# Performance work log

Measured on AMD Instinct MI355X. Metric: run time of the kernel, lower is better.

The kernel has to match this reference:

```python
import jax, jax.numpy as jnp
import numpy as np

KS = 3          # kernel size (forced by the view() shape constraint)
STRIDE = 1
PAD = 1
DIL = 1
K = KS * KS     # 9 taps


def _bilinear_sample(x, py, px):
    """x: [B,C,Hin,Win]; py,px: [B,C,K,H,W] float sample coords.
    Zero padding outside bounds (torchvision DeformConv semantics:
    each corner contributes only if it lies inside the image)."""
    B, C, Hin, Win = x.shape
    y0 = jnp.floor(py)
    x0 = jnp.floor(px)
    wy1 = py - y0
    wx1 = px - x0
    wy0 = 1.0 - wy1
    wx0 = 1.0 - wx1
    xf = x.reshape(B, C, Hin * Win)

    def gather(yi, xi):
        valid = (yi >= 0) & (yi <= Hin - 1) & (xi >= 0) & (xi <= Win - 1)
        yc = jnp.clip(yi, 0, Hin - 1).astype(jnp.int32)
        xc = jnp.clip(xi, 0, Win - 1).astype(jnp.int32)
        flat = (yc * Win + xc).reshape(B, C, -1)
        g = jnp.take_along_axis(xf, flat, axis=2).reshape(yi.shape)
        return jnp.where(valid, g, 0.0)

    return (wy0 * wx0 * gather(y0, x0)
            + wy0 * wx1 * gather(y0, x0 + 1)
            + wy1 * wx0 * gather(y0 + 1, x0)
            + wy1 * wx1 * gather(y0 + 1, x0 + 1))


def setup_inputs() -> dict:
    key = jax.random.key(0)
    ks = jax.random.split(key, 5)
    B, C, H, W = 8, 64, 128, 128
    Cout = 64
    return {
        "x": jax.random.normal(ks[0], (B, C, H, W), dtype=jnp.float32),
        # depthwise offset conv: groups=C, out = 18*C -> weight (18C, 1, 3, 3)
        "offset_w": jax.random.normal(ks[1], (2 * K * C, 1, 3, 3), dtype=jnp.float32) * 0.05,
        "offset_b": jax.random.normal(ks[2], (2 * K * C,), dtype=jnp.float32) * 0.05,
        "deform_w": jax.random.normal(ks[3], (Cout, C, KS, KS), dtype=jnp.float32) * 0.05,
        "deform_b": jax.random.normal(ks[4], (Cout,), dtype=jnp.float32) * 0.05,
    }


def reference(x, offset_w, offset_b, deform_w, deform_b):
    B, C, H, W = x.shape
    Cout = deform_w.shape[0]

    # 1) depthwise offset conv (groups = in_channels)
    off = jax.lax.conv_general_dilated(
        x, offset_w, window_strides=(STRIDE, STRIDE),
        padding=((PAD, PAD), (PAD, PAD)), rhs_dilation=(DIL, DIL),
        feature_group_count=C,
        dimension_numbers=("NCHW", "OIHW", "NCHW"))
    off = off + offset_b[None, :, None, None]

    # 2) softmax over the full channel axis (dim=1 in torch)
    off = jax.nn.softmax(off, axis=1)

    # 3) torchvision offset layout: channel 2*(g*K + k) + {0:dy, 1:dx},
    #    deformable_groups = C (per-input-channel offsets)
    off = off.reshape(B, C, K, 2, H, W)
    dy = off[:, :, :, 0]   # [B,C,K,H,W]
    dx = off[:, :, :, 1]

    base_y = (jnp.arange(H, dtype=x.dtype) * STRIDE - PAD)   # [H]
    base_x = (jnp.arange(W, dtype=x.dtype) * STRIDE - PAD)   # [W]
    ky = (jnp.repeat(jnp.arange(KS), KS) * DIL).astype(x.dtype)  # [K]
    kx = (jnp.tile(jnp.arange(KS), KS) * DIL).astype(x.dtype)

    py = base_y[None, None, None, :, None] + ky[None, None, :, None, None] + dy
    px = base_x[None, None, None, None, :] + kx[None, None, :, None, None] + dx

    sampled = _bilinear_sample(x, py, px)                    # [B,C,K,H,W]

    # 4) weighted accumulation over (c_in, kernel tap)
    out = jnp.einsum("bckhw,ock->bohw", sampled, deform_w.reshape(Cout, C, K))
    return out + deform_b[None, :, None, None]
```

## Files before the change

### kernel.cpp

```cpp
#include <hip/hip_runtime.h>

#define B_    8
#define C_    64
#define H_    128
#define W_    128
#define K_    9
#define J_    18
#define COUT_ 64
#define TPX   16
#define CK    576
#define SROW  584
#define NW81  (C_ * 81)
#define L2E   1.4426950408889634f

typedef __attribute__((ext_vector_type(8))) short short8;
typedef __attribute__((ext_vector_type(4))) float float4v;
typedef __attribute__((ext_vector_type(2))) float f32x2;

__device__ __forceinline__ unsigned short f2bf(float f) {
    unsigned int u = __float_as_uint(f);
    u = u + 0x7fffu + ((u >> 16) & 1u);
    return (unsigned short)(u >> 16);
}

constexpr int TMAP[9] = {0, 1, 2, 7, 8, 9, 14, 15, 16};

__global__ __launch_bounds__(256)
void nchw_to_nhwc(const float* __restrict__ x, float* __restrict__ xt) {
    __shared__ float tile[64][65];
    const int bid = blockIdx.x;
    const int wt  = bid & 1;
    const int h   = (bid >> 1) & 127;
    const int b   = bid >> 8;
    const int w0  = wt << 6;
    const int q   = threadIdx.x >> 6;
    const int l   = threadIdx.x & 63;
    #pragma unroll
    for (int r = 0; r < 16; r++) {
        const int c = q * 16 + r;
        tile[c][l] = x[((size_t)(b * C_ + c) * H_ + h) * W_ + w0 + l];
    }
    __syncthreads();
    #pragma unroll
    for (int r = 0; r < 16; r++) {
        const int w = q * 16 + r;
        xt[((size_t)(b * H_ + h) * W_ + w0 + w) * C_ + l] = tile[l][w];
    }
}

__global__ __launch_bounds__(256)
void prep_weights(const float* __restrict__ dw, unsigned short* __restrict__ dwb,
                  const float* __restrict__ ow, unsigned int* __restrict__ owp) {
    const int bid = blockIdx.x;
    const int dwblocks = (CK * COUT_) / 256;
    if (bid < dwblocks) {
        const int i = bid * 256 + threadIdx.x;
        dwb[i] = f2bf(dw[i]);
    } else {
        const int i = (bid - dwblocks) * 256 + threadIdx.x;
        if (i < NW81) {
            const int c = i / 81, r = i - c * 81;
            const int k = r / 9,  t = r - k * 9;
            const float* s = ow + c * 162 + k * 18 + t;
            owp[i] = (unsigned int)f2bf(s[0] * L2E) |
                     ((unsigned int)f2bf(s[9] * L2E) << 16);
        }
    }
}

template<int T>
__device__ __forceinline__ void conv_steps(const unsigned int* __restrict__ owc,
                                           const float (&S)[28], f32x2 (&v2)[4][9]) {
    if constexpr (T < 81) {
        const unsigned int pw = owc[T];
        const f32x2 w2 = {__uint_as_float(pw << 16),
                          __uint_as_float(pw & 0xffff0000u)};
        constexpr int k = T / 9;
        constexpr int p = TMAP[T % 9];
        #pragma unroll
        for (int px = 0; px < 4; px++) {
            const float s = S[p + px];
            v2[px][k] = __builtin_elementwise_fma(w2, (f32x2){s, s}, v2[px][k]);
        }
        conv_steps<T + 1>(owc, S, v2);
    }
}

template<int I>
__device__ __forceinline__ void taps_px(const f32x2 (&w)[9], const float inv,
                                        const float (&S)[28],
                                        unsigned short* __restrict__ sb) {
    #pragma unroll
    for (int k = 0; k < 9; k++) {
        const float dy = w[k].x * inv;
        const float dx = w[k].y * inv;
        const int base = TMAP[k] + I;
        const float a  = S[base],     bb = S[base + 1];
        const float c  = S[base + 7], dd = S[base + 8];
        const float top = fmaf(dx, bb - a, a);
        const float bot = fmaf(dx, dd - c, c);
        sb[k] = f2bf(fmaf(dy, bot - top, top));
    }
}

template<bool NHWC, bool PREB, bool PREP>
__global__ __launch_bounds__(256, 3)
void dcn_fused(const float* __restrict__ xsrc,
               const float* __restrict__ ow,
               const unsigned int* __restrict__ owp,
               const float* __restrict__ ob,
               const float* __restrict__ dw,
               const unsigned short* __restrict__ dwb,
               const float* __restrict__ db,
               float* __restrict__ out) {
    static_assert(TPX * SROW * sizeof(unsigned short) <= NW81 * sizeof(unsigned int), "union");
    __shared__ __align__(16) unsigned int smem[NW81];
    unsigned int* ow_s = smem;
    unsigned short* sbuf = (unsigned short*)smem;

    const int tid  = threadIdx.x;
    const int wave = tid >> 6;
    const int lane = tid & 63;

    const int bid = blockIdx.x;
    const int b   = bid >> 10;
    const int rem = bid & 1023;
    const int h   = rem >> 3;
    const int w0  = (rem & 7) << 4;

    if (PREP) {
        #pragma unroll
        for (int i = 0; i < 21; i++) {
            const int idx = tid + i * 256;
            if (idx < NW81) ow_s[idx] = owp[idx];
        }
    } else {
        for (int i = tid; i < NW81; i += 256) {
            const int c = i / 81, r = i - c * 81;
            const int k = r / 9,  t = r - k * 9;
            const float* s = ow + c * 162 + k * 18 + t;
            ow_s[i] = (unsigned int)f2bf(s[0] * L2E) |
                      ((unsigned int)f2bf(s[9] * L2E) << 16);
        }
    }
    __syncthreads();

    const int wbase = w0 + (wave << 2);
    const unsigned int* owc = ow_s + lane * 81;

    float S[28];
    if (h >= 1 && h <= H_ - 3 && wbase >= 1 && wbase <= W_ - 6) {
        const float* p0 = NHWC
            ? xsrc + ((size_t)(b * H_ + (h - 1)) * W_ + (wbase - 1)) * C_ + lane
            : xsrc + ((size_t)(b * C_ + lane) * H_ + (h - 1)) * W_ + (wbase - 1);
        const int rs = NHWC ? (W_ * C_) : W_;
        const int cs = NHWC ? C_ : 1;
        #pragma unroll
        for (int r = 0; r < 4; r++)
            #pragma unroll
            for (int s = 0; s < 7; s++)
                S[r * 7 + s] = p0[r * rs + s * cs];
    } else {
        #pragma unroll
        for (int r = 0; r < 4; r++) {
            const int y = h - 1 + r;
            const bool yv = (unsigned)y < (unsigned)H_;
            #pragma unroll
            for (int s = 0; s < 7; s++) {
                const int xx = wbase - 1 + s;
                const bool ok = yv && ((unsigned)xx < (unsigned)W_);
                const float* p = NHWC
                    ? xsrc + ((size_t)(b * H_ + (y & 127)) * W_ + (xx & 127)) * C_ + lane
                    : xsrc + ((size_t)(b * C_ + lane) * H_ + (y & 127)) * W_ + (xx & 127);
                S[r * 7 + s] = ok ? *p : 0.0f;
            }
        }
    }

    f32x2 v2[4][9];
    const float2* obp = (const float2*)(ob + lane * J_);
    #pragma unroll
    for (int p = 0; p < 9; p++) {
        const float2 f = obp[p];
        const f32x2 b2 = {f.x * L2E, f.y * L2E};
        v2[0][p] = b2; v2[1][p] = b2; v2[2][p] = b2; v2[3][p] = b2;
    }
    conv_steps<0>(owc, S, v2);

    float psum[4];
    #pragma unroll
    for (int px = 0; px < 4; px++) {
        float s = 0.0f;
        #pragma unroll
        for (int k = 0; k < 9; k++) {
            f32x2 e;
            e.x = __builtin_amdgcn_exp2f(v2[px][k].x);
            e.y = __builtin_amdgcn_exp2f(v2[px][k].y);
            v2[px][k] = e;
            s += e.x + e.y;
        }
        psum[px] = s;
    }

    __syncthreads();

    #pragma unroll
    for (int px = 0; px < 4; px++) psum[px] += __shfl_xor(psum[px], 32, 64);
#define RED_LEVEL(PAT) do { \
        const float r0_ = __uint_as_float((unsigned)__builtin_amdgcn_ds_swizzle((int)__float_as_uint(psum[0]), (PAT))); \
        const float r1_ = __uint_as_float((unsigned)__builtin_amdgcn_ds_swizzle((int)__float_as_uint(psum[1]), (PAT))); \
        const float r2_ = __uint_as_float((unsigned)__builtin_amdgcn_ds_swizzle((int)__float_as_uint(psum[2]), (PAT))); \
        const float r3_ = __uint_as_float((unsigned)__builtin_amdgcn_ds_swizzle((int)__float_as_uint(psum[3]), (PAT))); \
        psum[0] += r0_; psum[1] += r1_; psum[2] += r2_; psum[3] += r3_; \
    } while (0)
    RED_LEVEL(0x401F);
    RED_LEVEL(0x201F);
    RED_LEVEL(0x101F);
    RED_LEVEL(0x081F);
    RED_LEVEL(0x041F);
#undef RED_LEVEL

    const float inv0 = __builtin_amdgcn_rcpf(psum[0]);
    const float inv1 = __builtin_amdgcn_rcpf(psum[1]);
    const float inv2 = __builtin_amdgcn_rcpf(psum[2]);
    const float inv3 = __builtin_amdgcn_rcpf(psum[3]);

    unsigned short* sb = sbuf + (wave << 2) * SROW + lane * K_;
    taps_px<0>(v2[0], inv0, S, sb);
    taps_px<1>(v2[1], inv1, S, sb + SROW);
    taps_px<2>(v2[2], inv2, S, sb + 2 * SROW);
    taps_px<3>(v2[3], inv3, S, sb + 3 * SROW);

    __syncthreads();

    const int quad = lane >> 4;
    const int o    = (wave << 4) + (lane & 15);
    float4v acc = {0.f, 0.f, 0.f, 0.f};
    const unsigned short* arow = sbuf + (lane & 15) * SROW + quad * 8;
    #pragma unroll
    for (int t = 0; t < 18; t++) {
        short8 afrag = *(const short8*)(arow + t * 32);
        short8 bfrag;
        if (PREB) {
            bfrag = *(const short8*)(dwb + (size_t)o * CK + quad * 8 + t * 32);
        } else {
            const float* brow = dw + (size_t)o * CK + quad * 8 + t * 32;
            float4 b0 = *(const float4*)brow;
            float4 b1 = *(const float4*)(brow + 4);
            union { short8 s8; unsigned short u[8]; } bfu;
            bfu.u[0] = f2bf(b0.x); bfu.u[1] = f2bf(b0.y); bfu.u[2] = f2bf(b0.z); bfu.u[3] = f2bf(b0.w);
            bfu.u[4] = f2bf(b1.x); bfu.u[5] = f2bf(b1.y); bfu.u[6] = f2bf(b1.z); bfu.u[7] = f2bf(b1.w);
            bfrag = bfu.s8;
        }
        acc = __builtin_amdgcn_mfma_f32_16x16x32_bf16(afrag, bfrag, acc, 0, 0, 0);
    }
    const float bias = db[o];
    const int px0 = quad << 2;
    float4 res;
    res.x = acc[0] + bias; res.y = acc[1] + bias; res.z = acc[2] + bias; res.w = acc[3] + bias;
    *(float4*)(out + ((size_t)(b * COUT_ + o) * H_ + h) * W_ + w0 + px0) = res;
}

extern "C" void kernel_launch(void* const* d_in, const int* in_sizes, int n_in,
                              void* d_out, int out_size, void* d_ws, size_t ws_size,
                              hipStream_t stream) {
    (void)in_sizes; (void)n_in; (void)out_size;
    const float* x  = (const float*)d_in[0];
    const float* ow = (const float*)d_in[1];
    const float* ob = (const float*)d_in[2];
    const float* dw = (const float*)d_in[3];
    const float* db = (const float*)d_in[4];
    float* outp = (float*)d_out;

    const size_t xbytes  = (size_t)B_ * C_ * H_ * W_ * sizeof(float);
    const size_t dwbytes = (size_t)CK * COUT_ * sizeof(unsigned short);
    const size_t owbytes = (size_t)NW81 * sizeof(unsigned int);
    const dim3 grid(B_ * H_ * (W_ / TPX)), blk(256);
    const int dwblocks = (CK * COUT_) / 256;
    const int owblocks = (NW81 + 255) / 256;

    if (ws_size >= xbytes + dwbytes + owbytes) {
        float* xt = (float*)d_ws;
        unsigned short* dwb = (unsigned short*)((char*)d_ws + xbytes);
        unsigned int* owp = (unsigned int*)((char*)d_ws + xbytes + dwbytes);
        nchw_to_nhwc<<<dim3(B_ * H_ * 2), blk, 0, stream>>>(x, xt);
        prep_weights<<<dim3(dwblocks + owblocks), blk, 0, stream>>>(dw, dwb, ow, owp);
        dcn_fused<true, true, true><<<grid, blk, 0, stream>>>(xt, ow, owp, ob, dw, dwb, db, outp);
    } else if (ws_size >= xbytes + dwbytes) {
        float* xt = (float*)d_ws;
        unsigned short* dwb = (unsigned short*)((char*)d_ws + xbytes);
        nchw_to_nhwc<<<dim3(B_ * H_ * 2), blk, 0, stream>>>(x, xt);
        prep_weights<<<dim3(dwblocks), blk, 0, stream>>>(dw, dwb, nullptr, nullptr);
        dcn_fused<true, true, false><<<grid, blk, 0, stream>>>(xt, ow, nullptr, ob, dw, dwb, db, outp);
    } else if (ws_size >= xbytes) {
        float* xt = (float*)d_ws;
        nchw_to_nhwc<<<dim3(B_ * H_ * 2), blk, 0, stream>>>(x, xt);
        dcn_fused<true, false, false><<<grid, blk, 0, stream>>>(xt, ow, nullptr, ob, dw, nullptr, db, outp);
    } else {
        dcn_fused<false, false, false><<<grid, blk, 0, stream>>>(x, ow, nullptr, ob, dw, nullptr, db, outp);
    }
}
```

Baseline: 201.6 us.

## Process four tiles per block with prefetched input strips and separate LDS buffers

Each block now loops over four 16-pixel tiles (64 pixels) instead of one, so the per-block staging of the offset-conv weights into LDS is amortised over four times more work. The input strip for the next tile is loaded into a second register array while the current tile computes its exp/softmax, overlapping global loads with math. The weight and sample buffers get separate LDS arrays rather than a union, and block indices are swizzled across batches. This costs more registers and LDS per block, which may reduce occupancy, and the grid shrinks to 2048 blocks.

```diff
diff --git a/kernel.cpp b/kernel.cpp
--- a/kernel.cpp
+++ b/kernel.cpp
@@ -8,6 +8,7 @@
 #define J_    18
 #define COUT_ 64
 #define TPX   16
+#define TILES 4
 #define CK    576
 #define SROW  584
 #define NW81  (C_ * 81)
@@ -103,52 +104,10 @@
     }
 }
 
-template<bool NHWC, bool PREB, bool PREP>
-__global__ __launch_bounds__(256, 3)
-void dcn_fused(const float* __restrict__ xsrc,
-               const float* __restrict__ ow,
-               const unsigned int* __restrict__ owp,
-               const float* __restrict__ ob,
-               const float* __restrict__ dw,
-               const unsigned short* __restrict__ dwb,
-               const float* __restrict__ db,
-               float* __restrict__ out) {
-    static_assert(TPX * SROW * sizeof(unsigned short) <= NW81 * sizeof(unsigned int), "union");
-    __shared__ __align__(16) unsigned int smem[NW81];
-    unsigned int* ow_s = smem;
-    unsigned short* sbuf = (unsigned short*)smem;
-
-    const int tid  = threadIdx.x;
-    const int wave = tid >> 6;
-    const int lane = tid & 63;
-
-    const int bid = blockIdx.x;
-    const int b   = bid >> 10;
-    const int rem = bid & 1023;
-    const int h   = rem >> 3;
-    const int w0  = (rem & 7) << 4;
-
-    if (PREP) {
-        #pragma unroll
-        for (int i = 0; i < 21; i++) {
-            const int idx = tid + i * 256;
-            if (idx < NW81) ow_s[idx] = owp[idx];
-        }
-    } else {
-        for (int i = tid; i < NW81; i += 256) {
-            const int c = i / 81, r = i - c * 81;
-            const int k = r / 9,  t = r - k * 9;
-            const float* s = ow + c * 162 + k * 18 + t;
-            ow_s[i] = (unsigned int)f2bf(s[0] * L2E) |
-                      ((unsigned int)f2bf(s[9] * L2E) << 16);
-        }
-    }
-    __syncthreads();
-
-    const int wbase = w0 + (wave << 2);
-    const unsigned int* owc = ow_s + lane * 81;
-
-    float S[28];
+template<bool NHWC>
+__device__ __forceinline__ void load_strip(const float* __restrict__ xsrc,
+                                           int b, int h, int wbase, int lane,
+                                           float (&S)[28]) {
     if (h >= 1 && h <= H_ - 3 && wbase >= 1 && wbase <= W_ - 6) {
         const float* p0 = NHWC
             ? xsrc + ((size_t)(b * H_ + (h - 1)) * W_ + (wbase - 1)) * C_ + lane
@@ -176,36 +135,96 @@
             }
         }
     }
-
-    f32x2 v2[4][9];
+}
+
+template<bool NHWC, bool PREB, bool PREP>
+__global__ __launch_bounds__(256, 3)
+void dcn_fused(const float* __restrict__ xsrc,
+               const float* __restrict__ ow,
+               const unsigned int* __restrict__ owp,
+               const float* __restrict__ ob,
+               const float* __restrict__ dw,
+               const unsigned short* __restrict__ dwb,
+               const float* __restrict__ db,
+               float* __restrict__ out) {
+    __shared__ __align__(16) unsigned int ow_s[NW81];
+    __shared__ __align__(16) unsigned short sbuf[TPX * SROW];
+
+    const int tid  = threadIdx.x;
+    const int wave = tid >> 6;
+    const int lane = tid & 63;
+
+    const int bid     = blockIdx.x;
+    const int logical = (bid & 7) * 256 + (bid >> 3);
+    const int b       = logical >> 8;
+    const int h       = (logical >> 1) & 127;
+    const int w0base  = (logical & 1) << 6;
+
+    if (PREP) {
+        #pragma unroll
+        for (int i = 0; i < 21; i++) {
+            const int idx = tid + i * 256;
+            if (idx < NW81) ow_s[idx] = owp[idx];
+        }
+    } else {
+        for (int i = tid; i < NW81; i += 256) {
+            const int c = i / 81, r = i - c * 81;
+            const int k = r / 9,  t = r - k * 9;
+            const float* s = ow + c * 162 + k * 18 + t;
+            ow_s[i] = (unsigned int)f2bf(s[0] * L2E) |
+                      ((unsigned int)f2bf(s[9] * L2E) << 16);
+        }
+    }
+
+    const int quad = lane >> 4;
+    const int o    = (wave << 4) + (lane & 15);
+    const unsigned short* arow  = sbuf + (lane & 15) * SROW + quad * 8;
+    const unsigned short* bbase = PREB ? (dwb + (size_t)o * CK + quad * 8) : nullptr;
+    const float* brow0 = PREB ? nullptr : (dw + (size_t)o * CK + quad * 8);
+    const float bias = db[o];
+    float* outrow = out + ((size_t)(b * COUT_ + o) * H_ + h) * W_;
+
+    const unsigned int* owc = ow_s + lane * 81;
     const float2* obp = (const float2*)(ob + lane * J_);
-    #pragma unroll
-    for (int p = 0; p < 9; p++) {
-        const float2 f = obp[p];
-        const f32x2 b2 = {f.x * L2E, f.y * L2E};
-        v2[0][p] = b2; v2[1][p] = b2; v2[2][p] = b2; v2[3][p] = b2;
-    }
-    conv_steps<0>(owc, S, v2);
-
-    float psum[4];
-    #pragma unroll
-    for (int px = 0; px < 4; px++) {
-        float s = 0.0f;
-        #pragma unroll
-        for (int k = 0; k < 9; k++) {
-            f32x2 e;
-            e.x = __builtin_amdgcn_exp2f(v2[px][k].x);
-            e.y = __builtin_amdgcn_exp2f(v2[px][k].y);
-            v2[px][k] = e;
-            s += e.x + e.y;
-        }
-        psum[px] = s;
-    }
 
     __syncthreads();
 
-    #pragma unroll
-    for (int px = 0; px < 4; px++) psum[px] += __shfl_xor(psum[px], 32, 64);
+    float S[28], S2[28];
+    load_strip<NHWC>(xsrc, b, h, w0base + (wave << 2), lane, S);
+
+    #pragma unroll 1
+    for (int tt = 0; tt < TILES; tt++) {
+        const int w0 = w0base + (tt << 4);
+
+        f32x2 v2[4][9];
+        #pragma unroll
+        for (int p = 0; p < 9; p++) {
+            const float2 f = obp[p];
+            const f32x2 b2 = {f.x * L2E, f.y * L2E};
+            v2[0][p] = b2; v2[1][p] = b2; v2[2][p] = b2; v2[3][p] = b2;
+        }
+        conv_steps<0>(owc, S, v2);
+
+        if (tt + 1 < TILES)
+            load_strip<NHWC>(xsrc, b, h, w0base + ((tt + 1) << 4) + (wave << 2), lane, S2);
+
+        float psum[4];
+        #pragma unroll
+        for (int px = 0; px < 4; px++) {
+            float s = 0.0f;
+            #pragma unroll
+            for (int k = 0; k < 9; k++) {
+                f32x2 e;
+                e.x = __builtin_amdgcn_exp2f(v2[px][k].x);
+                e.y = __builtin_amdgcn_exp2f(v2[px][k].y);
+                v2[px][k] = e;
+                s += e.x + e.y;
+            }
+            psum[px] = s;
+        }
+
+        #pragma unroll
+        for (int px = 0; px < 4; px++) psum[px] += __shfl_xor(psum[px], 32, 64);
 #define RED_LEVEL(PAT) do { \
         const float r0_ = __uint_as_float((unsigned)__builtin_amdgcn_ds_swizzle((int)__float_as_uint(psum[0]), (PAT))); \
         const float r1_ = __uint_as_float((unsigned)__builtin_amdgcn_ds_swizzle((int)__float_as_uint(psum[1]), (PAT))); \
@@ -213,52 +232,56 @@
         const float r3_ = __uint_as_float((unsigned)__builtin_amdgcn_ds_swizzle((int)__float_as_uint(psum[3]), (PAT))); \
         psum[0] += r0_; psum[1] += r1_; psum[2] += r2_; psum[3] += r3_; \
     } while (0)
-    RED_LEVEL(0x401F);
-    RED_LEVEL(0x201F);
-    RED_LEVEL(0x101F);
-    RED_LEVEL(0x081F);
-    RED_LEVEL(0x041F);
+        RED_LEVEL(0x401F);
+        RED_LEVEL(0x201F);
+        RED_LEVEL(0x101F);
+        RED_LEVEL(0x081F);
+        RED_LEVEL(0x041F);
 #undef RED_LEVEL
 
-    const float inv0 = __builtin_amdgcn_rcpf(psum[0]);
-    const float inv1 = __builtin_amdgcn_rcpf(psum[1]);
-    const float inv2 = __builtin_amdgcn_rcpf(psum[2]);
-    const float inv3 = __builtin_amdgcn_rcpf(psum[3]);
-
-    unsigned short* sb = sbuf + (wave << 2) * SROW + lane * K_;
-    taps_px<0>(v2[0], inv0, S, sb);
-    taps_px<1>(v2[1], inv1, S, sb + SROW);
-    taps_px<2>(v2[2], inv2, S, sb + 2 * SROW);
-    taps_px<3>(v2[3], inv3, S, sb + 3 * SROW);
-
-    __syncthreads();
-
-    const int quad = lane >> 4;
-    const int o    = (wave << 4) + (lane & 15);
-    float4v acc = {0.f, 0.f, 0.f, 0.f};
-    const unsigned short* arow = sbuf + (lane & 15) * SROW + quad * 8;
-    #pragma unroll
-    for (int t = 0; t < 18; t++) {
-        short8 afrag = *(const short8*)(arow + t * 32);
-        short8 bfrag;
-        if (PREB) {
-            bfrag = *(const short8*)(dwb + (size_t)o * CK + quad * 8 + t * 32);
-        } else {
-            const float* brow = dw + (size_t)o * CK + quad * 8 + t * 32;
-            float4 b0 = *(const float4*)brow;
-            float4 b1 = *(const float4*)(brow + 4);
-            union { short8 s8; unsigned short u[8]; } bfu;
-            bfu.u[0] = f2bf(b0.x); bfu.u[1] = f2bf(b0.y); bfu.u[2] = f2bf(b0.z); bfu.u[3] = f2bf(b0.w);
-            bfu.u[4] = f2bf(b1.x); bfu.u[5] = f2bf(b1.y); bfu.u[6] = f2bf(b1.z); bfu.u[7] = f2bf(b1.w);
-            bfrag = bfu.s8;
-        }
-        acc = __builtin_amdgcn_mfma_f32_16x16x32_bf16(afrag, bfrag, acc, 0, 0, 0);
-    }
-    const float bias = db[o];
-    const int px0 = quad << 2;
-    float4 res;
-    res.x = acc[0] + bias; res.y = acc[1] + bias; res.z = acc[2] + bias; res.w = acc[3] + bias;
-    *(float4*)(out + ((size_t)(b * COUT_ + o) * H_ + h) * W_ + w0 + px0) = res;
+        const float inv0 = __builtin_amdgcn_rcpf(psum[0]);
+        const float inv1 = __builtin_amdgcn_rcpf(psum[1]);
+        const float inv2 = __builtin_amdgcn_rcpf(psum[2]);
+        const float inv3 = __builtin_amdgcn_rcpf(psum[3]);
+
+        unsigned short* sb = sbuf + (wave << 2) * SROW + lane * K_;
+        taps_px<0>(v2[0], inv0, S, sb);
+        taps_px<1>(v2[1], inv1, S, sb + SROW);
+        taps_px<2>(v2[2], inv2, S, sb + 2 * SROW);
+        taps_px<3>(v2[3], inv3, S, sb + 3 * SROW);
+
+        __syncthreads();
+
+        float4v acc = {0.f, 0.f, 0.f, 0.f};
+        #pragma unroll
+        for (int t = 0; t < 18; t++) {
+            short8 afrag = *(const short8*)(arow + t * 32);
+            short8 bfrag;
+            if (PREB) {
+                bfrag = *(const short8*)(bbase + t * 32);
+            } else {
+                const float* brow = brow0 + t * 32;
+                float4 b0 = *(const float4*)brow;
+                float4 b1 = *(const float4*)(brow + 4);
+                union { short8 s8; unsigned short u[8]; } bfu;
+                bfu.u[0] = f2bf(b0.x); bfu.u[1] = f2bf(b0.y); bfu.u[2] = f2bf(b0.z); bfu.u[3] = f2bf(b0.w);
+                bfu.u[4] = f2bf(b1.x); bfu.u[5] = f2bf(b1.y); bfu.u[6] = f2bf(b1.z); bfu.u[7] = f2bf(b1.w);
+                bfrag = bfu.s8;
+            }
+            acc = __builtin_amdgcn_mfma_f32_16x16x32_bf16(afrag, bfrag, acc, 0, 0, 0);
+        }
+        float4 res;
+        res.x = acc[0] + bias; res.y = acc[1] + bias;
+        res.z = acc[2] + bias; res.w = acc[3] + bias;
+        *(float4*)(outrow + w0 + (quad << 2)) = res;
+
+        __syncthreads();
+
+        if (tt + 1 < TILES) {
+            #pragma unroll
+            for (int i = 0; i < 28; i++) S[i] = S2[i];
+        }
+    }
 }
 
 extern "C" void kernel_launch(void* const* d_in, const int* in_sizes, int n_in,
@@ -275,7 +298,7 @@
     const size_t xbytes  = (size_t)B_ * C_ * H_ * W_ * sizeof(float);
     const size_t dwbytes = (size_t)CK * COUT_ * sizeof(unsigned short);
     const size_t owbytes = (size_t)NW81 * sizeof(unsigned int);
-    const dim3 grid(B_ * H_ * (W_ / TPX)), blk(256);
+    const dim3 grid(B_ * H_ * 2), blk(256);
     const int dwblocks = (CK * COUT_) / 256;
     const int owblocks = (NW81 + 255) / 256;
 
```

After: 313.4 us. 55.5% more time.
